# Kernel optimization log

Measured on AMD Instinct MI355X. Metric: run time of the kernel, lower is better.

Reference implementation:

```python
import jax, jax.numpy as jnp
import numpy as np

N_NODES = 170000
N_EDGES = 1200000
F_IN, HID, N_CLS = 128, 64, 40
N_CONVS = 7  # num_layers - 1
ALPHA, THETA = 0.1, 0.5


def setup_inputs() -> dict:
    key = jax.random.key(0)
    ks = jax.random.split(key, 8)
    x = jax.random.normal(ks[0], (N_NODES, F_IN), dtype=jnp.float32)
    edge_src = jax.random.randint(ks[1], (N_EDGES,), 0, N_NODES, dtype=jnp.int32)
    edge_dst = jax.random.randint(ks[2], (N_EDGES,), 0, N_NODES, dtype=jnp.int32)
    # pre-normalized adjacency values (normalize=False in GCN2Conv)
    edge_weight = jax.random.uniform(ks[3], (N_EDGES,), dtype=jnp.float32)
    W_in = jax.random.normal(ks[4], (F_IN, HID), dtype=jnp.float32) / np.sqrt(F_IN)
    b_in = jnp.zeros((HID,), dtype=jnp.float32)
    conv_W = jax.random.normal(ks[5], (N_CONVS, HID, HID), dtype=jnp.float32) / np.sqrt(HID)
    W_out = jax.random.normal(ks[6], (HID, N_CLS), dtype=jnp.float32) / np.sqrt(HID)
    b_out = jnp.zeros((N_CLS,), dtype=jnp.float32)
    return {"x": x, "edge_src": edge_src, "edge_dst": edge_dst,
            "edge_weight": edge_weight, "W_in": W_in, "b_in": b_in,
            "conv_W": conv_W, "W_out": W_out, "b_out": b_out}


def reference(x, edge_src, edge_dst, edge_weight, W_in, b_in, conv_W, W_out, b_out):
    n = x.shape[0]
    h = jax.nn.relu(x @ W_in + b_in)          # [N, HID]
    x0 = h                                    # initial residual
    for l in range(conv_W.shape[0]):
        beta = float(np.log(THETA / (l + 1) + 1.0))
        # SpMM: adj_t @ h  (gather from source, weighted scatter-add to target)
        msg = h[edge_src] * edge_weight[:, None]             # [E, HID]
        agg = jax.ops.segment_sum(msg, edge_dst, num_segments=n)
        hh = (1.0 - ALPHA) * agg + ALPHA * x0                # initial residual mix
        h = jax.nn.relu((1.0 - beta) * hh + beta * (hh @ conv_W[l]))  # identity mapping
    out = h @ W_out + b_out
    return jax.nn.log_softmax(out, axis=-1)
```

## Files before the change

kernel.cpp:

```cpp
#include <hip/hip_runtime.h>
#include <math.h>

typedef _Float16 f16x8 __attribute__((ext_vector_type(8)));
typedef float f32x4 __attribute__((ext_vector_type(4)));

__device__ __forceinline__ float us2f(unsigned short u) {
  _Float16 h;
  __builtin_memcpy(&h, &u, 2);
  return (float)h;
}
__device__ __forceinline__ unsigned short f2us(float f) {
  _Float16 h = (_Float16)f;
  unsigned short u;
  __builtin_memcpy(&u, &h, 2);
  return u;
}

__device__ __forceinline__ float bcast(float v, int k) {
  return __int_as_float(__builtin_amdgcn_readlane(__float_as_int(v), k));
}

__global__ __launch_bounds__(256) void hist_k(const int* __restrict__ dst, int* __restrict__ deg,
                                              int E, int N) {
  int xcd = blockIdx.x & 7;
  int bid = blockIdx.x >> 3;
  int nb = gridDim.x >> 3;
  int R = (N + 7) >> 3;
  int lo = xcd * R;
  int hi = min(N, lo + R);
  for (int e = bid * blockDim.x + threadIdx.x; e < E; e += nb * blockDim.x) {
    int d = dst[e];
    if (d >= lo && d < hi) atomicAdd(&deg[d], 1);
  }
}

__global__ __launch_bounds__(1024) void scan1_k(const int* __restrict__ deg, int* __restrict__ rp,
                                                int* __restrict__ bsum, int n) {
  __shared__ int buf[2][1024];
  int tid = threadIdx.x;
  int i = blockIdx.x * 1024 + tid;
  int v = (i < n) ? deg[i] : 0;
  int pp = 0;
  buf[0][tid] = v;
  __syncthreads();
  for (int off = 1; off < 1024; off <<= 1) {
    int t = buf[pp][tid];
    if (tid >= off) t += buf[pp][tid - off];
    buf[pp ^ 1][tid] = t;
    pp ^= 1;
    __syncthreads();
  }
  int inc = buf[pp][tid];
  if (i < n) rp[i] = inc - v;
  if (tid == 1023) bsum[blockIdx.x] = inc;
}

__global__ __launch_bounds__(256) void scan2_k(int* __restrict__ bsum, int nb) {
  __shared__ int buf[2][256];
  int tid = threadIdx.x;
  int v = (tid < nb) ? bsum[tid] : 0;
  int pp = 0;
  buf[0][tid] = v;
  __syncthreads();
  for (int off = 1; off < 256; off <<= 1) {
    int t = buf[pp][tid];
    if (tid >= off) t += buf[pp][tid - off];
    buf[pp ^ 1][tid] = t;
    pp ^= 1;
    __syncthreads();
  }
  if (tid < nb) bsum[tid] = buf[pp][tid] - v;
}

__global__ __launch_bounds__(1024) void scan3_k(int* __restrict__ rp, int* __restrict__ cur,
                                                const int* __restrict__ bsum, int n, int E) {
  int i = blockIdx.x * 1024 + threadIdx.x;
  if (i < n) {
    int v = rp[i] + bsum[blockIdx.x];
    rp[i] = v;
    cur[i] = v;
  }
  if (i == 0) rp[n] = E;
}

__global__ __launch_bounds__(256) void scatter_k(const int* __restrict__ src, const int* __restrict__ dst,
                                                 const float* __restrict__ w, int* __restrict__ cur,
                                                 int2* __restrict__ edge, int E, int N) {
  int xcd = blockIdx.x & 7;
  int bid = blockIdx.x >> 3;
  int nb = gridDim.x >> 3;
  int R = (N + 7) >> 3;
  int lo = xcd * R;
  int hi = min(N, lo + R);
  for (int e = bid * blockDim.x + threadIdx.x; e < E; e += nb * blockDim.x) {
    int d = dst[e];
    if (d >= lo && d < hi) {
      int pos = atomicAdd(&cur[d], 1);
      edge[pos] = make_int2(src[e], __float_as_int(w[e]));
    }
  }
}

__global__ __launch_bounds__(256) void ingemm_k(const float* __restrict__ x, const float* __restrict__ Win,
                                                const float* __restrict__ bin, unsigned short* __restrict__ x0,
                                                int n) {
  int lane = threadIdx.x & 63;
  int wave = threadIdx.x >> 6;
  int col = lane & 15, grp = lane >> 4;
  f16x8 B[4][4];
#pragma unroll
  for (int c = 0; c < 4; ++c)
#pragma unroll
    for (int t = 0; t < 4; ++t) {
      f16x8 b;
#pragma unroll
      for (int j = 0; j < 8; ++j) b[j] = (_Float16)Win[(c * 32 + grp * 8 + j) * 64 + t * 16 + col];
      B[c][t] = b;
    }
  float bb[4];
#pragma unroll
  for (int t = 0; t < 4; ++t) bb[t] = bin[t * 16 + col];

  int node_base = (blockIdx.x * 4 + wave) * 16;
  if (node_base >= n) return;
  int arow = node_base + col;
  if (arow > n - 1) arow = n - 1;
  const float* xr = x + (size_t)arow * 128 + grp * 8;

  f32x4 acc[4];
  f32x4 z = {0.f, 0.f, 0.f, 0.f};
#pragma unroll
  for (int t = 0; t < 4; ++t) acc[t] = z;
#pragma unroll
  for (int c = 0; c < 4; ++c) {
    f32x4 lo = *(const f32x4*)(xr + c * 32);
    f32x4 hi = *(const f32x4*)(xr + c * 32 + 4);
    f16x8 a;
#pragma unroll
    for (int j = 0; j < 4; ++j) a[j] = (_Float16)lo[j];
#pragma unroll
    for (int j = 0; j < 4; ++j) a[4 + j] = (_Float16)hi[j];
#pragma unroll
    for (int t = 0; t < 4; ++t) acc[t] = __builtin_amdgcn_mfma_f32_16x16x32_f16(a, B[c][t], acc[t], 0, 0, 0);
  }
#pragma unroll
  for (int t = 0; t < 4; ++t)
#pragma unroll
    for (int r = 0; r < 4; ++r) {
      int node = node_base + grp * 4 + r;
      if (node < n) {
        float o = acc[t][r] + bb[t];
        x0[(size_t)node * 64 + t * 16 + col] = f2us(fmaxf(o, 0.f));
      }
    }
}

__global__ __launch_bounds__(256) void spmm_k(const ushort2* __restrict__ hin2,
                                              const ushort2* __restrict__ x02,
                                              const int* __restrict__ rp, const int2* __restrict__ edge,
                                              ushort2* __restrict__ hh2, int n) {
  int lane = threadIdx.x & 63;
  int wave = threadIdx.x >> 6;
  int half = lane >> 5;
  int sl = lane & 31;
  int S = gridDim.x * 8;
  for (int node = (blockIdx.x * 4 + wave) * 2 + half; node < n; node += S) {
    int beg = rp[node], end = rp[node + 1];
    ushort2 xv = x02[(size_t)node * 32 + sl];
    float ax = 0.f, ay = 0.f;
    for (int e = beg; e < end; e += 8) {
      int2 d[8];
#pragma unroll
      for (int j = 0; j < 8; ++j) d[j] = (e + j < end) ? edge[e + j] : make_int2(0, 0);
      ushort2 v[8];
#pragma unroll
      for (int j = 0; j < 8; ++j) v[j] = hin2[(size_t)d[j].x * 32 + sl];
#pragma unroll
      for (int j = 0; j < 8; ++j) {
        float w = __int_as_float(d[j].y);
        ax = fmaf(us2f(v[j].x), w, ax);
        ay = fmaf(us2f(v[j].y), w, ay);
      }
    }
    float hx = fmaf(0.9f, ax, 0.1f * us2f(xv.x));
    float hy = fmaf(0.9f, ay, 0.1f * us2f(xv.y));
    ushort2 o;
    o.x = f2us(hx);
    o.y = f2us(hy);
    hh2[(size_t)node * 32 + sl] = o;
  }
}

__global__ __launch_bounds__(256) void gemm_k(const unsigned short* __restrict__ hh,
                                              const float* __restrict__ W, unsigned short* __restrict__ hout,
                                              float beta, int n) {
  int lane = threadIdx.x & 63;
  int wave = threadIdx.x >> 6;
  int col = lane & 15, grp = lane >> 4;
  f16x8 B[2][4];
#pragma unroll
  for (int c = 0; c < 2; ++c)
#pragma unroll
    for (int t = 0; t < 4; ++t) {
      f16x8 b;
#pragma unroll
      for (int j = 0; j < 8; ++j) b[j] = (_Float16)W[(c * 32 + grp * 8 + j) * 64 + t * 16 + col];
      B[c][t] = b;
    }
  int node_base = (blockIdx.x * 4 + wave) * 16;
  if (node_base >= n) return;
  int arow = node_base + col;
  if (arow > n - 1) arow = n - 1;
  const unsigned short* rowp = hh + (size_t)arow * 64 + grp * 8;
  f16x8 A0 = *(const f16x8*)(rowp);
  f16x8 A1 = *(const f16x8*)(rowp + 32);

  f32x4 acc[4];
  f32x4 z = {0.f, 0.f, 0.f, 0.f};
#pragma unroll
  for (int t = 0; t < 4; ++t) acc[t] = z;
#pragma unroll
  for (int t = 0; t < 4; ++t) {
    acc[t] = __builtin_amdgcn_mfma_f32_16x16x32_f16(A0, B[0][t], acc[t], 0, 0, 0);
    acc[t] = __builtin_amdgcn_mfma_f32_16x16x32_f16(A1, B[1][t], acc[t], 0, 0, 0);
  }
  float ob = 1.f - beta;
#pragma unroll
  for (int t = 0; t < 4; ++t)
#pragma unroll
    for (int r = 0; r < 4; ++r) {
      int node = node_base + grp * 4 + r;
      if (node < n) {
        float hv = us2f(hh[(size_t)node * 64 + t * 16 + col]);
        float o = ob * hv + beta * acc[t][r];
        hout[(size_t)node * 64 + t * 16 + col] = f2us(fmaxf(o, 0.f));
      }
    }
}

__global__ __launch_bounds__(256) void out_k(const unsigned short* __restrict__ h,
                                             const float* __restrict__ Wout, const float* __restrict__ bout,
                                             float* __restrict__ out, int n) {
  int lane = threadIdx.x & 63;
  int wave = threadIdx.x >> 6;
  int S = gridDim.x * 4;
  float Wreg[64];
#pragma unroll
  for (int k = 0; k < 64; ++k) Wreg[k] = (lane < 40) ? Wout[k * 40 + lane] : 0.f;
  float bb = (lane < 40) ? bout[lane] : 0.f;
  int node = blockIdx.x * 4 + wave;
  if (node >= n) return;
  float hv = us2f(h[(size_t)node * 64 + lane]);
  for (; node < n; node += S) {
    int nn = node + S;
    float nhv = (nn < n) ? us2f(h[(size_t)nn * 64 + lane]) : 0.f;
    float d0 = 0.f, d1 = 0.f;
#pragma unroll
    for (int k = 0; k < 64; k += 2) {
      d0 = fmaf(bcast(hv, k), Wreg[k], d0);
      d1 = fmaf(bcast(hv, k + 1), Wreg[k + 1], d1);
    }
    float val = (lane < 40) ? (d0 + d1 + bb) : -INFINITY;
    float m = val;
#pragma unroll
    for (int mask = 32; mask >= 1; mask >>= 1) m = fmaxf(m, __shfl_xor(m, mask, 64));
    float p = (lane < 40) ? expf(val - m) : 0.f;
    float s = p;
#pragma unroll
    for (int mask = 32; mask >= 1; mask >>= 1) s += __shfl_xor(s, mask, 64);
    float ls = val - m - logf(s);
    if (lane < 40) out[(size_t)node * 40 + lane] = ls;
    hv = nhv;
  }
}

extern "C" void kernel_launch(void* const* d_in, const int* in_sizes, int n_in,
                              void* d_out, int out_size, void* d_ws, size_t ws_size,
                              hipStream_t stream) {
  const float* x = (const float*)d_in[0];
  const int* esrc = (const int*)d_in[1];
  const int* edst = (const int*)d_in[2];
  const float* ew = (const float*)d_in[3];
  const float* Win = (const float*)d_in[4];
  const float* bin = (const float*)d_in[5];
  const float* convW = (const float*)d_in[6];
  const float* Wout = (const float*)d_in[7];
  const float* bout = (const float*)d_in[8];
  float* out = (float*)d_out;

  const int N = in_sizes[0] / 128;
  const int E = in_sizes[1];
  const int NC = in_sizes[6] / (64 * 64);

  char* ws = (char*)d_ws;
  size_t off = 0;
  auto alloc = [&](size_t b) {
    void* p = ws + off;
    off += (b + 255) & ~(size_t)255;
    return p;
  };
  unsigned short* x0 = (unsigned short*)alloc((size_t)N * 64 * 2);
  unsigned short* ha = (unsigned short*)alloc((size_t)N * 64 * 2);
  unsigned short* hb = (unsigned short*)alloc((size_t)N * 64 * 2);
  unsigned short* hhb = (unsigned short*)alloc((size_t)N * 64 * 2);
  int* deg = (int*)alloc((size_t)N * 4);
  int* rp = (int*)alloc((size_t)(N + 1) * 4);
  int* cur = (int*)alloc((size_t)N * 4);
  int* bsum = (int*)alloc(1024);
  int2* edge = (int2*)alloc((size_t)E * 8);

  hipMemsetAsync(deg, 0, (size_t)N * 4, stream);
  hist_k<<<2048, 256, 0, stream>>>(edst, deg, E, N);
  int nb = (N + 1023) / 1024;
  scan1_k<<<nb, 1024, 0, stream>>>(deg, rp, bsum, N);
  scan2_k<<<1, 256, 0, stream>>>(bsum, nb);
  scan3_k<<<nb, 1024, 0, stream>>>(rp, cur, bsum, N, E);
  scatter_k<<<2048, 256, 0, stream>>>(esrc, edst, ew, cur, edge, E, N);

  int gblocks = (N + 63) / 64;
  ingemm_k<<<gblocks, 256, 0, stream>>>(x, Win, bin, x0, N);

  const unsigned short* hin = x0;
  unsigned short* bufs[2] = {ha, hb};
  for (int l = 0; l < NC; ++l) {
    float beta = logf(0.5f / (float)(l + 1) + 1.0f);
    unsigned short* ho = bufs[l & 1];
    spmm_k<<<2048, 256, 0, stream>>>((const ushort2*)hin, (const ushort2*)x0, rp, edge, (ushort2*)hhb, N);
    gemm_k<<<gblocks, 256, 0, stream>>>(hhb, convW + (size_t)l * 64 * 64, ho, beta, N);
    hin = ho;
  }
  out_k<<<2048, 256, 0, stream>>>(hin, Wout, bout, out, N);
}
```

Baseline: 668.9 us.

## Widen SpMM gathers to 8-byte loads and move output GEMM to MFMA

```diff
diff --git a/kernel.cpp b/kernel.cpp
--- a/kernel.cpp
+++ b/kernel.cpp
@@ -14,10 +14,6 @@
   unsigned short u;
   __builtin_memcpy(&u, &h, 2);
   return u;
-}
-
-__device__ __forceinline__ float bcast(float v, int k) {
-  return __int_as_float(__builtin_amdgcn_readlane(__float_as_int(v), k));
 }
 
 __global__ __launch_bounds__(256) void hist_k(const int* __restrict__ dst, int* __restrict__ deg,
@@ -155,39 +151,41 @@
     }
 }
 
-__global__ __launch_bounds__(256) void spmm_k(const ushort2* __restrict__ hin2,
-                                              const ushort2* __restrict__ x02,
+__global__ __launch_bounds__(256) void spmm_k(const ushort4* __restrict__ hin4,
+                                              const ushort4* __restrict__ x04,
                                               const int* __restrict__ rp, const int2* __restrict__ edge,
-                                              ushort2* __restrict__ hh2, int n) {
+                                              ushort4* __restrict__ hh4, int n) {
   int lane = threadIdx.x & 63;
   int wave = threadIdx.x >> 6;
-  int half = lane >> 5;
-  int sl = lane & 31;
-  int S = gridDim.x * 8;
-  for (int node = (blockIdx.x * 4 + wave) * 2 + half; node < n; node += S) {
+  int q = lane >> 4;
+  int sl = lane & 15;
+  int S = gridDim.x * 16;
+  for (int node = (blockIdx.x * 4 + wave) * 4 + q; node < n; node += S) {
     int beg = rp[node], end = rp[node + 1];
-    ushort2 xv = x02[(size_t)node * 32 + sl];
-    float ax = 0.f, ay = 0.f;
+    ushort4 xv = x04[(size_t)node * 16 + sl];
+    float a0 = 0.f, a1 = 0.f, a2 = 0.f, a3 = 0.f;
     for (int e = beg; e < end; e += 8) {
       int2 d[8];
 #pragma unroll
       for (int j = 0; j < 8; ++j) d[j] = (e + j < end) ? edge[e + j] : make_int2(0, 0);
-      ushort2 v[8];
-#pragma unroll
-      for (int j = 0; j < 8; ++j) v[j] = hin2[(size_t)d[j].x * 32 + sl];
+      ushort4 v[8];
+#pragma unroll
+      for (int j = 0; j < 8; ++j) v[j] = hin4[(size_t)d[j].x * 16 + sl];
 #pragma unroll
       for (int j = 0; j < 8; ++j) {
         float w = __int_as_float(d[j].y);
-        ax = fmaf(us2f(v[j].x), w, ax);
-        ay = fmaf(us2f(v[j].y), w, ay);
+        a0 = fmaf(us2f(v[j].x), w, a0);
+        a1 = fmaf(us2f(v[j].y), w, a1);
+        a2 = fmaf(us2f(v[j].z), w, a2);
+        a3 = fmaf(us2f(v[j].w), w, a3);
       }
     }
-    float hx = fmaf(0.9f, ax, 0.1f * us2f(xv.x));
-    float hy = fmaf(0.9f, ay, 0.1f * us2f(xv.y));
-    ushort2 o;
-    o.x = f2us(hx);
-    o.y = f2us(hy);
-    hh2[(size_t)node * 32 + sl] = o;
+    ushort4 o;
+    o.x = f2us(fmaf(0.9f, a0, 0.1f * us2f(xv.x)));
+    o.y = f2us(fmaf(0.9f, a1, 0.1f * us2f(xv.y)));
+    o.z = f2us(fmaf(0.9f, a2, 0.1f * us2f(xv.z)));
+    o.w = f2us(fmaf(0.9f, a3, 0.1f * us2f(xv.w)));
+    hh4[(size_t)node * 16 + sl] = o;
   }
 }
 
@@ -243,34 +241,59 @@
                                              float* __restrict__ out, int n) {
   int lane = threadIdx.x & 63;
   int wave = threadIdx.x >> 6;
-  int S = gridDim.x * 4;
-  float Wreg[64];
-#pragma unroll
-  for (int k = 0; k < 64; ++k) Wreg[k] = (lane < 40) ? Wout[k * 40 + lane] : 0.f;
-  float bb = (lane < 40) ? bout[lane] : 0.f;
-  int node = blockIdx.x * 4 + wave;
-  if (node >= n) return;
-  float hv = us2f(h[(size_t)node * 64 + lane]);
-  for (; node < n; node += S) {
-    int nn = node + S;
-    float nhv = (nn < n) ? us2f(h[(size_t)nn * 64 + lane]) : 0.f;
-    float d0 = 0.f, d1 = 0.f;
-#pragma unroll
-    for (int k = 0; k < 64; k += 2) {
-      d0 = fmaf(bcast(hv, k), Wreg[k], d0);
-      d1 = fmaf(bcast(hv, k + 1), Wreg[k + 1], d1);
-    }
-    float val = (lane < 40) ? (d0 + d1 + bb) : -INFINITY;
-    float m = val;
-#pragma unroll
-    for (int mask = 32; mask >= 1; mask >>= 1) m = fmaxf(m, __shfl_xor(m, mask, 64));
-    float p = (lane < 40) ? expf(val - m) : 0.f;
-    float s = p;
-#pragma unroll
-    for (int mask = 32; mask >= 1; mask >>= 1) s += __shfl_xor(s, mask, 64);
-    float ls = val - m - logf(s);
-    if (lane < 40) out[(size_t)node * 40 + lane] = ls;
-    hv = nhv;
+  int col = lane & 15, grp = lane >> 4;
+  f16x8 B[2][3];
+#pragma unroll
+  for (int c = 0; c < 2; ++c)
+#pragma unroll
+    for (int t = 0; t < 3; ++t) {
+      int cls = t * 16 + col;
+      f16x8 b;
+#pragma unroll
+      for (int j = 0; j < 8; ++j) b[j] = (cls < 40) ? (_Float16)Wout[(c * 32 + grp * 8 + j) * 40 + cls] : (_Float16)0.f;
+      B[c][t] = b;
+    }
+  float bb[3];
+#pragma unroll
+  for (int t = 0; t < 3; ++t) {
+    int cls = t * 16 + col;
+    bb[t] = (cls < 40) ? bout[cls] : 0.f;
+  }
+  int node_base = (blockIdx.x * 4 + wave) * 16;
+  if (node_base >= n) return;
+  int arow = node_base + col;
+  if (arow > n - 1) arow = n - 1;
+  const unsigned short* rowp = h + (size_t)arow * 64 + grp * 8;
+  f16x8 A0 = *(const f16x8*)(rowp);
+  f16x8 A1 = *(const f16x8*)(rowp + 32);
+
+  f32x4 acc[3];
+  f32x4 z = {0.f, 0.f, 0.f, 0.f};
+#pragma unroll
+  for (int t = 0; t < 3; ++t) acc[t] = z;
+#pragma unroll
+  for (int t = 0; t < 3; ++t) {
+    acc[t] = __builtin_amdgcn_mfma_f32_16x16x32_f16(A0, B[0][t], acc[t], 0, 0, 0);
+    acc[t] = __builtin_amdgcn_mfma_f32_16x16x32_f16(A1, B[1][t], acc[t], 0, 0, 0);
+  }
+#pragma unroll
+  for (int r = 0; r < 4; ++r) {
+    int node = node_base + grp * 4 + r;
+    float v0 = acc[0][r] + bb[0];
+    float v1 = acc[1][r] + bb[1];
+    float v2 = (32 + col < 40) ? (acc[2][r] + bb[2]) : -INFINITY;
+    float m = fmaxf(fmaxf(v0, v1), v2);
+#pragma unroll
+    for (int mask = 1; mask <= 8; mask <<= 1) m = fmaxf(m, __shfl_xor(m, mask, 64));
+    float p = expf(v0 - m) + expf(v1 - m) + ((32 + col < 40) ? expf(v2 - m) : 0.f);
+#pragma unroll
+    for (int mask = 1; mask <= 8; mask <<= 1) p += __shfl_xor(p, mask, 64);
+    float ml = m + logf(p);
+    if (node < n) {
+      out[(size_t)node * 40 + col] = v0 - ml;
+      out[(size_t)node * 40 + 16 + col] = v1 - ml;
+      if (32 + col < 40) out[(size_t)node * 40 + 32 + col] = v2 - ml;
+    }
   }
 }
 
@@ -325,9 +348,9 @@
   for (int l = 0; l < NC; ++l) {
     float beta = logf(0.5f / (float)(l + 1) + 1.0f);
     unsigned short* ho = bufs[l & 1];
-    spmm_k<<<2048, 256, 0, stream>>>((const ushort2*)hin, (const ushort2*)x0, rp, edge, (ushort2*)hhb, N);
+    spmm_k<<<2048, 256, 0, stream>>>((const ushort4*)hin, (const ushort4*)x0, rp, edge, (ushort4*)hhb, N);
     gemm_k<<<gblocks, 256, 0, stream>>>(hhb, convW + (size_t)l * 64 * 64, ho, beta, N);
     hin = ho;
   }
-  out_k<<<2048, 256, 0, stream>>>(hin, Wout, bout, out, N);
-}
+  out_k<<<gblocks, 256, 0, stream>>>(hin, Wout, bout, out, N);
+}
```

After: 561.7 us. 16.0% less time.
